# Optimization experiments

Hardware: AMD Instinct MI355X
Metric: run time of the kernel (lower is better)

The kernel has to match this reference:

```python
import jax, jax.numpy as jnp
import numpy as np

NUM_GRAPHS = 1024
DIM = 64
IN_DIM = 25
PROC_STEPS = 3


def setup_inputs() -> dict:
    key = jax.random.key(0)
    ks = jax.random.split(key, 14)
    N, E = 100000, 1600000
    s = 0.1
    x = jax.random.normal(ks[0], (N, IN_DIM), jnp.float32)
    edge_index = jax.random.randint(ks[1], (2, E), 0, N, dtype=jnp.int64)
    batch = jnp.sort(jax.random.randint(ks[2], (N,), 0, NUM_GRAPHS, dtype=jnp.int64))
    return {
        "x": x,
        "edge_index": edge_index,
        "batch": batch,
        # lin0: 25 -> 64
        "lin0_W": jax.random.normal(ks[3], (IN_DIM, DIM), jnp.float32) * s,
        "lin0_b": jnp.zeros((DIM,), jnp.float32),
        # GINConv nn: 64 -> 64
        "gin_W": jax.random.normal(ks[4], (DIM, DIM), jnp.float32) * s,
        "gin_b": jnp.zeros((DIM,), jnp.float32),
        # Set2Set LSTM: input 2*dim -> hidden dim, torch gate order (i, f, g, o)
        "W_ih": jax.random.normal(ks[5], (4 * DIM, 2 * DIM), jnp.float32) * s,
        "W_hh": jax.random.normal(ks[6], (4 * DIM, DIM), jnp.float32) * s,
        "b_ih": jnp.zeros((4 * DIM,), jnp.float32),
        "b_hh": jnp.zeros((4 * DIM,), jnp.float32),
        # lin1: 128 -> 64, lin2: 64 -> 1
        "lin1_W": jax.random.normal(ks[7], (2 * DIM, DIM), jnp.float32) * s,
        "lin1_b": jnp.zeros((DIM,), jnp.float32),
        "lin2_W": jax.random.normal(ks[8], (DIM, 1), jnp.float32) * s,
        "lin2_b": jnp.zeros((1,), jnp.float32),
    }


def reference(x, edge_index, batch, lin0_W, lin0_b, gin_W, gin_b,
              W_ih, W_hh, b_ih, b_hh, lin1_W, lin1_b, lin2_W, lin2_b):
    N = x.shape[0]
    B = NUM_GRAPHS
    # lin0 + relu
    h0 = jax.nn.relu(x @ lin0_W + lin0_b)  # [N, 64]
    # GINConv (eps=0): out = nn((1+eps)*x + sum_{j in N(i)} x_j), then relu
    src, dst = edge_index[0], edge_index[1]
    aggr = jax.ops.segment_sum(h0[src], dst, num_segments=N)  # scatter-add [N, 64]
    h1 = jax.nn.relu((h0 + aggr) @ gin_W + gin_b)  # [N, 64]
    # Set2Set pooling: 3 steps of LSTM + softmax attention over each graph
    q_star = jnp.zeros((B, 2 * DIM), h1.dtype)
    h = jnp.zeros((B, DIM), h1.dtype)
    c = jnp.zeros((B, DIM), h1.dtype)
    for _ in range(PROC_STEPS):
        gates = q_star @ W_ih.T + h @ W_hh.T + b_ih + b_hh  # [B, 4*64]
        i_g, f_g, g_g, o_g = jnp.split(gates, 4, axis=-1)
        c = jax.nn.sigmoid(f_g) * c + jax.nn.sigmoid(i_g) * jnp.tanh(g_g)
        h = jax.nn.sigmoid(o_g) * jnp.tanh(c)
        q = h  # query [B, 64]
        e = jnp.sum(h1 * q[batch], axis=-1)  # [N]
        e_max = jax.ops.segment_max(e, batch, num_segments=B)
        a_un = jnp.exp(e - e_max[batch])
        denom = jax.ops.segment_sum(a_un, batch, num_segments=B)
        denom = jnp.where(denom == 0, 1.0, denom)
        a = a_un / denom[batch]  # per-graph softmax over nodes
        r = jax.ops.segment_sum(a[:, None] * h1, batch, num_segments=B)  # [B, 64]
        q_star = jnp.concatenate([q, r], axis=-1)  # [B, 128]
    out = jax.nn.relu(q_star @ lin1_W + lin1_b)
    out = out @ lin2_W + lin2_b  # [B, 1]
    return out.reshape(-1)
```

## Files before the change

### kernel.cpp

```cpp
#include <hip/hip_runtime.h>
#include <hip/hip_fp16.h>
#include <math.h>

#define DIM 64
#define IN_DIM 25
#define B_GRAPHS 1024
#define STEPS 3
#define MAXDEG 64
#define GPB 2
#define VCAP 16
#define BSHIFT 7
#define NBUCK_MAX 1024
#define BCAP 3072
#define CHUNK_A 4096

typedef _Float16 half8 __attribute__((ext_vector_type(8)));
typedef float    f32x4 __attribute__((ext_vector_type(4)));

__device__ __forceinline__ float wave_sum(float v) {
    #pragma unroll
    for (int o = 32; o > 0; o >>= 1) v += __shfl_xor(v, o, 64);
    return v;
}

__global__ void prepA_kernel(const int* __restrict__ ei, int E,
                             int* __restrict__ gcur,
                             unsigned* __restrict__ arena, int nbuck) {
    __shared__ int hist[NBUCK_MAX];
    int tid = threadIdx.x;
    for (int t = tid; t < nbuck; t += 256) hist[t] = 0;
    __syncthreads();
    int e0 = blockIdx.x * CHUNK_A;
    int dstr[16], lofs[16];
    #pragma unroll
    for (int k = 0; k < 16; ++k) {
        int e = e0 + k * 256 + tid;
        dstr[k] = -1;
        if (e < E) {
            int d = ei[E + e];
            dstr[k] = d;
            lofs[k] = atomicAdd(&hist[d >> BSHIFT], 1);
        }
    }
    __syncthreads();
    for (int t = tid; t < nbuck; t += 256)
        hist[t] = atomicAdd(&gcur[t], hist[t]);
    __syncthreads();
    #pragma unroll
    for (int k = 0; k < 16; ++k) {
        int d = dstr[k];
        if (d >= 0) {
            int e = e0 + k * 256 + tid;
            unsigned src = (unsigned)ei[e];
            int bk = d >> BSHIFT;
            int pos = hist[bk] + lofs[k];
            if (pos < BCAP)
                arena[(size_t)bk * BCAP + pos] =
                    (src << BSHIFT) | (unsigned)(d & ((1 << BSHIFT) - 1));
        }
    }
}

__global__ void prepB_kernel(const float* __restrict__ x,
                             const float* __restrict__ W,
                             const float* __restrict__ b,
                             __half* __restrict__ h0h,
                             const int* __restrict__ batch, int N,
                             const unsigned* __restrict__ arena,
                             const int* __restrict__ gcur,
                             int* __restrict__ cnt, int* __restrict__ csr,
                             int* __restrict__ startb, int* __restrict__ endb,
                             int nbuck, int nbL) {
    int bi = blockIdx.x;
    if (bi < nbuck) {
        int tid = threadIdx.x;
        __shared__ int cur[1 << BSHIFT];
        __shared__ int stage[(1 << BSHIFT) * MAXDEG];
        for (int t = tid; t < (1 << BSHIFT); t += 256) cur[t] = 0;
        __syncthreads();
        int nE = gcur[bi];
        if (nE > BCAP) nE = BCAP;
        int base = bi << BSHIFT;
        const unsigned* ap = arena + (size_t)bi * BCAP;
        for (int i = tid; i < nE; i += 256) {
            unsigned pk = ap[i];
            int dl  = pk & ((1 << BSHIFT) - 1);
            int src = pk >> BSHIFT;
            int pos = atomicAdd(&cur[dl], 1);
            if (pos < MAXDEG) {
                int slot = (pos & 3) * 16 + (pos >> 2);
                stage[dl * MAXDEG + slot] = src;
            }
        }
        __syncthreads();
        int rows = N - base;
        if (rows > (1 << BSHIFT)) rows = 1 << BSHIFT;
        if (rows < 0) rows = 0;
        const int4* s4 = (const int4*)stage;
        int4* g4 = (int4*)(csr + (size_t)base * MAXDEG);
        for (int f = tid; f < rows * 16; f += 256) g4[f] = s4[f];
        for (int t = tid; t < rows; t += 256)
            cnt[base + t] = cur[t] < MAXDEG ? cur[t] : MAXDEG;
    } else if (bi < nbuck + nbL) {
        int grp  = threadIdx.x >> 6;
        int lane = threadIdx.x & 63;
        int n = (bi - nbuck) * 4 + grp;
        if (n >= N) return;
        float acc = b[lane];
        const float* xr = x + (size_t)n * IN_DIM;
        #pragma unroll
        for (int k = 0; k < IN_DIM; ++k)
            acc += xr[k] * W[k * DIM + lane];
        h0h[(size_t)n * DIM + lane] = __float2half(fmaxf(acc, 0.f));
    } else {
        int i = (bi - nbuck - nbL) * 256 + threadIdx.x;
        if (i >= N) return;
        int g = batch[i];
        if (i == 0) {
            startb[g] = 0;
        } else if (batch[i - 1] != g) {
            startb[g] = i;
            endb[batch[i - 1]] = i;
        }
        if (i == N - 1) endb[g] = N;
    }
}

__global__ void gin_gather_kernel(const __half* __restrict__ h0h,
                                  const int* __restrict__ cnt,
                                  const int* __restrict__ csr,
                                  const float* __restrict__ W,
                                  const float* __restrict__ bias,
                                  __half* __restrict__ h1h, int N) {
    int wid  = threadIdx.x >> 6;
    int lane = threadIdx.x & 63;
    int sub  = lane & 15;
    int quad = lane >> 4;
    int nbase = blockIdx.x * 16;
    __shared__ __align__(16) __half agg[16][72];

    half8 bfrag0, bfrag1;
    {
        int cb = wid * 16 + sub;
        #pragma unroll
        for (int j = 0; j < 8; ++j) {
            bfrag0[j] = (_Float16)W[(quad * 8 + j) * DIM + cb];
            bfrag1[j] = (_Float16)W[(32 + quad * 8 + j) * DIM + cb];
        }
    }
    float bias_l = bias[wid * 16 + sub];

    #pragma unroll
    for (int t = 0; t < 4; ++t) {
        int n = nbase + t * 4 + wid;
        if (n < N) {
            int d = cnt[n];
            const int4* crow = (const int4*)(csr + (size_t)n * MAXDEG + quad * 16);
            int4 c0 = crow[0];
            float4 a0 = {0.f, 0.f, 0.f, 0.f};
            float4 a1 = {0.f, 0.f, 0.f, 0.f};

            bool v0 = (0 + quad) < d,  v1 = (4 + quad) < d;
            bool v2 = (8 + quad) < d,  v3 = (12 + quad) < d;
            int i0 = v0 ? c0.x : 0, i1 = v1 ? c0.y : 0;
            int i2 = v2 ? c0.z : 0, i3 = v3 ? c0.w : 0;
            uint2 r0 = *(const uint2*)(h0h + (size_t)i0 * DIM + 4 * sub);
            uint2 r1 = *(const uint2*)(h0h + (size_t)i1 * DIM + 4 * sub);
            uint2 r2 = *(const uint2*)(h0h + (size_t)i2 * DIM + 4 * sub);
            uint2 r3 = *(const uint2*)(h0h + (size_t)i3 * DIM + 4 * sub);
            #define ACC8(r, v, A)                                              \
                if (v) {                                                       \
                    __half2 ua = *reinterpret_cast<__half2*>(&(r).x);          \
                    __half2 ub = *reinterpret_cast<__half2*>(&(r).y);          \
                    float2 fa = __half22float2(ua), fb = __half22float2(ub);   \
                    A.x += fa.x; A.y += fa.y; A.z += fb.x; A.w += fb.y;        \
                }
            ACC8(r0, v0, a0) ACC8(r1, v1, a1) ACC8(r2, v2, a0) ACC8(r3, v3, a1)

            if (d > 16) {
                int4 c1 = crow[1];
                bool v4 = (16 + quad) < d, v5 = (20 + quad) < d;
                bool v6 = (24 + quad) < d, v7 = (28 + quad) < d;
                int i4 = v4 ? c1.x : 0, i5 = v5 ? c1.y : 0;
                int i6 = v6 ? c1.z : 0, i7 = v7 ? c1.w : 0;
                uint2 r4 = *(const uint2*)(h0h + (size_t)i4 * DIM + 4 * sub);
                uint2 r5 = *(const uint2*)(h0h + (size_t)i5 * DIM + 4 * sub);
                uint2 r6 = *(const uint2*)(h0h + (size_t)i6 * DIM + 4 * sub);
                uint2 r7 = *(const uint2*)(h0h + (size_t)i7 * DIM + 4 * sub);
                ACC8(r4, v4, a0) ACC8(r5, v5, a1) ACC8(r6, v6, a0) ACC8(r7, v7, a1)
            }
            if (d > 32) {
                int4 c2 = crow[2];
                int4 c3 = crow[3];
                bool w0 = (32 + quad) < d, w1 = (36 + quad) < d;
                bool w2 = (40 + quad) < d, w3 = (44 + quad) < d;
                bool w4 = (48 + quad) < d, w5 = (52 + quad) < d;
                bool w6 = (56 + quad) < d, w7 = (60 + quad) < d;
                int k0 = w0 ? c2.x : 0, k1 = w1 ? c2.y : 0;
                int k2 = w2 ? c2.z : 0, k3 = w3 ? c2.w : 0;
                int k4 = w4 ? c3.x : 0, k5 = w5 ? c3.y : 0;
                int k6 = w6 ? c3.z : 0, k7 = w7 ? c3.w : 0;
                uint2 t0 = *(const uint2*)(h0h + (size_t)k0 * DIM + 4 * sub);
                uint2 t1 = *(const uint2*)(h0h + (size_t)k1 * DIM + 4 * sub);
                uint2 t2 = *(const uint2*)(h0h + (size_t)k2 * DIM + 4 * sub);
                uint2 t3 = *(const uint2*)(h0h + (size_t)k3 * DIM + 4 * sub);
                uint2 t4 = *(const uint2*)(h0h + (size_t)k4 * DIM + 4 * sub);
                uint2 t5 = *(const uint2*)(h0h + (size_t)k5 * DIM + 4 * sub);
                uint2 t6 = *(const uint2*)(h0h + (size_t)k6 * DIM + 4 * sub);
                uint2 t7 = *(const uint2*)(h0h + (size_t)k7 * DIM + 4 * sub);
                ACC8(t0, w0, a0) ACC8(t1, w1, a1) ACC8(t2, w2, a0) ACC8(t3, w3, a1)
                ACC8(t4, w4, a0) ACC8(t5, w5, a1) ACC8(t6, w6, a0) ACC8(t7, w7, a1)
            }
            #undef ACC8

            float4 a;
            a.x = a0.x + a1.x; a.y = a0.y + a1.y;
            a.z = a0.z + a1.z; a.w = a0.w + a1.w;
            a.x += __shfl_xor(a.x, 16, 64); a.y += __shfl_xor(a.y, 16, 64);
            a.z += __shfl_xor(a.z, 16, 64); a.w += __shfl_xor(a.w, 16, 64);
            a.x += __shfl_xor(a.x, 32, 64); a.y += __shfl_xor(a.y, 32, 64);
            a.z += __shfl_xor(a.z, 32, 64); a.w += __shfl_xor(a.w, 32, 64);
            if (quad == 0) {
                const __half2* p = (const __half2*)(h0h + (size_t)n * DIM + 4 * sub);
                float2 f0 = __half22float2(p[0]), f1 = __half22float2(p[1]);
                a.x += f0.x; a.y += f0.y; a.z += f1.x; a.w += f1.y;
                __half2* dp = (__half2*)&agg[t * 4 + wid][4 * sub];
                dp[0] = __floats2half2_rn(a.x, a.y);
                dp[1] = __floats2half2_rn(a.z, a.w);
            }
        }
    }
    __syncthreads();

    half8 afrag0 = *(const half8*)&agg[sub][quad * 8];
    half8 afrag1 = *(const half8*)&agg[sub][32 + quad * 8];
    f32x4 acc = {0.f, 0.f, 0.f, 0.f};
    acc = __builtin_amdgcn_mfma_f32_16x16x32_f16(afrag0, bfrag0, acc, 0, 0, 0);
    acc = __builtin_amdgcn_mfma_f32_16x16x32_f16(afrag1, bfrag1, acc, 0, 0, 0);
    #pragma unroll
    for (int r = 0; r < 4; ++r) {
        int n = nbase + quad * 4 + r;
        if (n < N) {
            float v = fmaxf(acc[r] + bias_l, 0.f);
            h1h[(size_t)n * DIM + wid * 16 + sub] = __float2half(v);
        }
    }
}

__global__ __launch_bounds__(256)
void set2set_fused_kernel(const __half* __restrict__ h1h,
                          const float* __restrict__ W_ih,
                          const float* __restrict__ W_hh,
                          const float* __restrict__ b_ih,
                          const float* __restrict__ b_hh,
                          const int* __restrict__ startb,
                          const int* __restrict__ endb,
                          const float* __restrict__ lin1_W,
                          const float* __restrict__ lin1_b,
                          const float* __restrict__ lin2_W,
                          const float* __restrict__ lin2_b,
                          float* __restrict__ out) {
    int g0  = blockIdx.x * GPB;
    int tid = threadIdx.x;
    __shared__ __align__(16) float qsbuf[GPB][2 * DIM];
    __shared__ float csbuf[GPB][DIM];
    __shared__ float gatesL[GPB][4 * DIM];
    __shared__ float pmax[GPB][2];
    __shared__ float pden[GPB][2];
    __shared__ __align__(16) float4 pr[GPB][2][16];

    int wid  = tid >> 6;
    int myg  = wid >> 1;
    int wh   = wid & 1;
    int lane = tid & 63;
    int stg  = startb[g0 + myg];
    int cntg = endb[g0 + myg] - stg;
    if (cntg < 0) cntg = 0;

    for (int f = tid; f < GPB * 2 * DIM; f += 256) ((float*)qsbuf)[f] = 0.f;
    for (int f = tid; f < GPB * DIM; f += 256) ((float*)csbuf)[f] = 0.f;
    float bias_t = b_ih[tid] + b_hh[tid];
    __syncthreads();

    int sub   = lane & 15;
    int jslot = lane >> 4;
    int i0    = wh * 4 + jslot;

    for (int step = 0; step < STEPS; ++step) {
        {
            float a0 = bias_t, a1 = bias_t;
            const float4* wi = (const float4*)(W_ih + (size_t)tid * 2 * DIM);
            const float4* q0 = (const float4*)qsbuf[0];
            const float4* q1 = (const float4*)qsbuf[1];
            #pragma unroll 8
            for (int k = 0; k < 2 * DIM / 4; ++k) {
                float4 w = wi[k];
                float4 v0 = q0[k], v1 = q1[k];
                a0 += w.x * v0.x + w.y * v0.y + w.z * v0.z + w.w * v0.w;
                a1 += w.x * v1.x + w.y * v1.y + w.z * v1.z + w.w * v1.w;
            }
            const float4* wh4 = (const float4*)(W_hh + (size_t)tid * DIM);
            #pragma unroll 8
            for (int k = 0; k < DIM / 4; ++k) {
                float4 w = wh4[k];
                float4 v0 = q0[k], v1 = q1[k];
                a0 += w.x * v0.x + w.y * v0.y + w.z * v0.z + w.w * v0.w;
                a1 += w.x * v1.x + w.y * v1.y + w.z * v1.z + w.w * v1.w;
            }
            gatesL[0][tid] = a0; gatesL[1][tid] = a1;
        }
        __syncthreads();
        if (tid < GPB * DIM) {
            int g = tid >> 6, d = tid & 63;
            float ig = gatesL[g][d];
            float fg = gatesL[g][DIM + d];
            float gg = gatesL[g][2 * DIM + d];
            float og = gatesL[g][3 * DIM + d];
            float si = 1.f / (1.f + __expf(-ig));
            float sf = 1.f / (1.f + __expf(-fg));
            float so = 1.f / (1.f + __expf(-og));
            float cn = sf * csbuf[g][d] + si * tanhf(gg);
            float hn = so * tanhf(cn);
            csbuf[g][d] = cn;
            qsbuf[g][d] = hn;
        }
        __syncthreads();

        const float4 q4 = *(const float4*)(&qsbuf[myg][4 * sub]);

        float  pc[VCAP];
        float4 vc[VCAP];
        float gmax = -INFINITY;
        #pragma unroll
        for (int it = 0; it < VCAP; ++it) {
            int i = i0 + it * 8;
            bool vd = i < cntg;
            int r = vd ? (stg + i) : stg;
            const __half2* p = (const __half2*)(h1h + (size_t)r * DIM + 4 * sub);
            float2 f0 = __half22float2(p[0]), f1 = __half22float2(p[1]);
            float4 v; v.x = f0.x; v.y = f0.y; v.z = f1.x; v.w = f1.y;
            float pd = v.x * q4.x + v.y * q4.y + v.z * q4.z + v.w * q4.w;
            pd += __shfl_xor(pd, 1, 64);
            pd += __shfl_xor(pd, 2, 64);
            pd += __shfl_xor(pd, 4, 64);
            pd += __shfl_xor(pd, 8, 64);
            pd = vd ? pd : -INFINITY;
            pc[it] = pd;
            vc[it] = v;
            gmax = fmaxf(gmax, pd);
        }
        for (int i = i0 + VCAP * 8; i < cntg; i += 8) {
            const __half2* p =
                (const __half2*)(h1h + (size_t)(stg + i) * DIM + 4 * sub);
            float2 f0 = __half22float2(p[0]), f1 = __half22float2(p[1]);
            float pd = f0.x * q4.x + f0.y * q4.y + f1.x * q4.z + f1.y * q4.w;
            pd += __shfl_xor(pd, 1, 64);
            pd += __shfl_xor(pd, 2, 64);
            pd += __shfl_xor(pd, 4, 64);
            pd += __shfl_xor(pd, 8, 64);
            gmax = fmaxf(gmax, pd);
        }
        gmax = fmaxf(gmax, __shfl_xor(gmax, 16, 64));
        gmax = fmaxf(gmax, __shfl_xor(gmax, 32, 64));
        if (lane == 0) pmax[myg][wh] = gmax;
        __syncthreads();
        float m = fmaxf(fmaxf(pmax[myg][0], pmax[myg][1]), -1e30f);

        float4 racc = {0.f, 0.f, 0.f, 0.f};
        float den = 0.f;
        #pragma unroll
        for (int it = 0; it < VCAP; ++it) {
            float w = __expf(pc[it] - m);
            if (sub == 0) den += w;
            racc.x += w * vc[it].x; racc.y += w * vc[it].y;
            racc.z += w * vc[it].z; racc.w += w * vc[it].w;
        }
        for (int i = i0 + VCAP * 8; i < cntg; i += 8) {
            const __half2* p =
                (const __half2*)(h1h + (size_t)(stg + i) * DIM + 4 * sub);
            float2 f0 = __half22float2(p[0]), f1 = __half22float2(p[1]);
            float pd = f0.x * q4.x + f0.y * q4.y + f1.x * q4.z + f1.y * q4.w;
            pd += __shfl_xor(pd, 1, 64);
            pd += __shfl_xor(pd, 2, 64);
            pd += __shfl_xor(pd, 4, 64);
            pd += __shfl_xor(pd, 8, 64);
            float w = __expf(pd - m);
            if (sub == 0) den += w;
            racc.x += w * f0.x; racc.y += w * f0.y;
            racc.z += w * f1.x; racc.w += w * f1.y;
        }
        racc.x += __shfl_xor(racc.x, 16, 64); racc.y += __shfl_xor(racc.y, 16, 64);
        racc.z += __shfl_xor(racc.z, 16, 64); racc.w += __shfl_xor(racc.w, 16, 64);
        racc.x += __shfl_xor(racc.x, 32, 64); racc.y += __shfl_xor(racc.y, 32, 64);
        racc.z += __shfl_xor(racc.z, 32, 64); racc.w += __shfl_xor(racc.w, 32, 64);
        den += __shfl_xor(den, 16, 64);
        den += __shfl_xor(den, 32, 64);
        if (jslot == 0) pr[myg][wh][sub] = racc;
        if (lane == 0) pden[myg][wh] = den;
        __syncthreads();
        if (wh == 0 && jslot == 0) {
            float4 rA = pr[myg][0][sub];
            float4 rB = pr[myg][1][sub];
            float dt = pden[myg][0] + pden[myg][1];
            if (dt == 0.f) dt = 1.f;
            float4 rv;
            rv.x = (rA.x + rB.x) / dt; rv.y = (rA.y + rB.y) / dt;
            rv.z = (rA.z + rB.z) / dt; rv.w = (rA.w + rB.w) / dt;
            *(float4*)(&qsbuf[myg][DIM + 4 * sub]) = rv;
        }
        __syncthreads();
    }

    if (wh == 0) {
        float acc = lin1_b[lane];
        const float* qv = qsbuf[myg];
        #pragma unroll 8
        for (int k = 0; k < 2 * DIM; ++k)
            acc += qv[k] * lin1_W[k * DIM + lane];
        acc = fmaxf(acc, 0.f);
        float v = acc * lin2_W[lane];
        v = wave_sum(v);
        if (lane == 0) out[g0 + myg] = v + lin2_b[0];
    }
}

extern "C" void kernel_launch(void* const* d_in, const int* in_sizes, int n_in,
                              void* d_out, int out_size, void* d_ws, size_t ws_size,
                              hipStream_t stream) {
    const float* x      = (const float*)d_in[0];
    const int*   ei     = (const int*)d_in[1];
    const int*   batch  = (const int*)d_in[2];
    const float* lin0_W = (const float*)d_in[3];
    const float* lin0_b = (const float*)d_in[4];
    const float* gin_W  = (const float*)d_in[5];
    const float* gin_b  = (const float*)d_in[6];
    const float* W_ih   = (const float*)d_in[7];
    const float* W_hh   = (const float*)d_in[8];
    const float* b_ih   = (const float*)d_in[9];
    const float* b_hh   = (const float*)d_in[10];
    const float* lin1_W = (const float*)d_in[11];
    const float* lin1_b = (const float*)d_in[12];
    const float* lin2_W = (const float*)d_in[13];
    const float* lin2_b = (const float*)d_in[14];
    float* out = (float*)d_out;

    const int N = in_sizes[2];
    const int E = in_sizes[1] / 2;

    char* ws = (char*)d_ws;
    size_t off = 0;
    auto take = [&](size_t bytes) -> char* {
        char* p = ws + off;
        off += (bytes + 255) & ~(size_t)255;
        return p;
    };
    int nbuck = (N + (1 << BSHIFT) - 1) >> BSHIFT;

    __half*   h0h   = (__half*)take((size_t)N * DIM * 2);
    __half*   h1h   = (__half*)take((size_t)N * DIM * 2);
    int*      csr   = (int*)take((size_t)N * MAXDEG * 4);
    unsigned* arena = (unsigned*)take((size_t)nbuck * BCAP * 4);
    int*      cnt   = (int*)take((size_t)N * 4);
    int* startb = (int*)take((size_t)B_GRAPHS * 4);
    int* endb   = (int*)take((size_t)B_GRAPHS * 4);
    int* gcur   = (int*)take((size_t)NBUCK_MAX * 4);
    size_t zero_bytes = (size_t)((char*)gcur - (char*)startb) + NBUCK_MAX * 4;
    hipMemsetAsync(startb, 0, zero_bytes, stream);

    int nb4   = (N + 3) / 4;
    int nb16  = (N + 15) / 16;
    int nb256 = (N + 255) / 256;
    int fillB = (E + CHUNK_A - 1) / CHUNK_A;

    hipLaunchKernelGGL(prepA_kernel, dim3(fillB), dim3(256), 0, stream,
                       ei, E, gcur, arena, nbuck);
    hipLaunchKernelGGL(prepB_kernel, dim3(nbuck + nb4 + nb256), dim3(256), 0, stream,
                       x, lin0_W, lin0_b, h0h, batch, N,
                       arena, gcur, cnt, csr, startb, endb, nbuck, nb4);
    hipLaunchKernelGGL(gin_gather_kernel, dim3(nb16), dim3(256), 0, stream,
                       h0h, cnt, csr, gin_W, gin_b, h1h, N);
    hipLaunchKernelGGL(set2set_fused_kernel, dim3(B_GRAPHS / GPB), dim3(256), 0, stream,
                       h1h, W_ih, W_hh, b_ih, b_hh, startb, endb,
                       lin1_W, lin1_b, lin2_W, lin2_b, out);
}
```

Baseline: 262.3 us.

## Fuse CSR build into GIN gather and merge edge bucketing with lin0

```diff
diff --git a/kernel.cpp b/kernel.cpp
--- a/kernel.cpp
+++ b/kernel.cpp
@@ -23,88 +23,55 @@
     return v;
 }
 
-__global__ void prepA_kernel(const int* __restrict__ ei, int E,
-                             int* __restrict__ gcur,
-                             unsigned* __restrict__ arena, int nbuck) {
-    __shared__ int hist[NBUCK_MAX];
-    int tid = threadIdx.x;
-    for (int t = tid; t < nbuck; t += 256) hist[t] = 0;
-    __syncthreads();
-    int e0 = blockIdx.x * CHUNK_A;
-    int dstr[16], lofs[16];
-    #pragma unroll
-    for (int k = 0; k < 16; ++k) {
-        int e = e0 + k * 256 + tid;
-        dstr[k] = -1;
-        if (e < E) {
-            int d = ei[E + e];
-            dstr[k] = d;
-            lofs[k] = atomicAdd(&hist[d >> BSHIFT], 1);
-        }
-    }
-    __syncthreads();
-    for (int t = tid; t < nbuck; t += 256)
-        hist[t] = atomicAdd(&gcur[t], hist[t]);
-    __syncthreads();
-    #pragma unroll
-    for (int k = 0; k < 16; ++k) {
-        int d = dstr[k];
-        if (d >= 0) {
-            int e = e0 + k * 256 + tid;
-            unsigned src = (unsigned)ei[e];
-            int bk = d >> BSHIFT;
-            int pos = hist[bk] + lofs[k];
-            if (pos < BCAP)
-                arena[(size_t)bk * BCAP + pos] =
-                    (src << BSHIFT) | (unsigned)(d & ((1 << BSHIFT) - 1));
-        }
-    }
-}
-
-__global__ void prepB_kernel(const float* __restrict__ x,
+__global__ void prepA_kernel(const float* __restrict__ x,
                              const float* __restrict__ W,
                              const float* __restrict__ b,
                              __half* __restrict__ h0h,
+                             const int* __restrict__ ei, int E,
                              const int* __restrict__ batch, int N,
-                             const unsigned* __restrict__ arena,
-                             const int* __restrict__ gcur,
-                             int* __restrict__ cnt, int* __restrict__ csr,
+                             int* __restrict__ gcur,
+                             unsigned* __restrict__ arena,
                              int* __restrict__ startb, int* __restrict__ endb,
-                             int nbuck, int nbL) {
+                             int fillB, int nbL, int nbuck) {
     int bi = blockIdx.x;
-    if (bi < nbuck) {
+    if (bi < fillB) {
+        __shared__ int hist[NBUCK_MAX];
         int tid = threadIdx.x;
-        __shared__ int cur[1 << BSHIFT];
-        __shared__ int stage[(1 << BSHIFT) * MAXDEG];
-        for (int t = tid; t < (1 << BSHIFT); t += 256) cur[t] = 0;
-        __syncthreads();
-        int nE = gcur[bi];
-        if (nE > BCAP) nE = BCAP;
-        int base = bi << BSHIFT;
-        const unsigned* ap = arena + (size_t)bi * BCAP;
-        for (int i = tid; i < nE; i += 256) {
-            unsigned pk = ap[i];
-            int dl  = pk & ((1 << BSHIFT) - 1);
-            int src = pk >> BSHIFT;
-            int pos = atomicAdd(&cur[dl], 1);
-            if (pos < MAXDEG) {
-                int slot = (pos & 3) * 16 + (pos >> 2);
-                stage[dl * MAXDEG + slot] = src;
-            }
-        }
-        __syncthreads();
-        int rows = N - base;
-        if (rows > (1 << BSHIFT)) rows = 1 << BSHIFT;
-        if (rows < 0) rows = 0;
-        const int4* s4 = (const int4*)stage;
-        int4* g4 = (int4*)(csr + (size_t)base * MAXDEG);
-        for (int f = tid; f < rows * 16; f += 256) g4[f] = s4[f];
-        for (int t = tid; t < rows; t += 256)
-            cnt[base + t] = cur[t] < MAXDEG ? cur[t] : MAXDEG;
-    } else if (bi < nbuck + nbL) {
+        for (int t = tid; t < nbuck; t += 256) hist[t] = 0;
+        __syncthreads();
+        int e0 = bi * CHUNK_A;
+        int dstr[16], lofs[16];
+        #pragma unroll
+        for (int k = 0; k < 16; ++k) {
+            int e = e0 + k * 256 + tid;
+            dstr[k] = -1;
+            if (e < E) {
+                int d = ei[E + e];
+                dstr[k] = d;
+                lofs[k] = atomicAdd(&hist[d >> BSHIFT], 1);
+            }
+        }
+        __syncthreads();
+        for (int t = tid; t < nbuck; t += 256)
+            hist[t] = atomicAdd(&gcur[t], hist[t]);
+        __syncthreads();
+        #pragma unroll
+        for (int k = 0; k < 16; ++k) {
+            int d = dstr[k];
+            if (d >= 0) {
+                int e = e0 + k * 256 + tid;
+                unsigned src = (unsigned)ei[e];
+                int bk = d >> BSHIFT;
+                int pos = hist[bk] + lofs[k];
+                if (pos < BCAP)
+                    arena[(size_t)bk * BCAP + pos] =
+                        (src << BSHIFT) | (unsigned)(d & ((1 << BSHIFT) - 1));
+            }
+        }
+    } else if (bi < fillB + nbL) {
         int grp  = threadIdx.x >> 6;
         int lane = threadIdx.x & 63;
-        int n = (bi - nbuck) * 4 + grp;
+        int n = (bi - fillB) * 4 + grp;
         if (n >= N) return;
         float acc = b[lane];
         const float* xr = x + (size_t)n * IN_DIM;
@@ -113,7 +80,7 @@
             acc += xr[k] * W[k * DIM + lane];
         h0h[(size_t)n * DIM + lane] = __float2half(fmaxf(acc, 0.f));
     } else {
-        int i = (bi - nbuck - nbL) * 256 + threadIdx.x;
+        int i = (bi - fillB - nbL) * 256 + threadIdx.x;
         if (i >= N) return;
         int g = batch[i];
         if (i == 0) {
@@ -126,18 +93,26 @@
     }
 }
 
-__global__ void gin_gather_kernel(const __half* __restrict__ h0h,
-                                  const int* __restrict__ cnt,
-                                  const int* __restrict__ csr,
-                                  const float* __restrict__ W,
-                                  const float* __restrict__ bias,
-                                  __half* __restrict__ h1h, int N) {
-    int wid  = threadIdx.x >> 6;
-    int lane = threadIdx.x & 63;
+__global__ void gin_fused_kernel(const __half* __restrict__ h0h,
+                                 const unsigned* __restrict__ arena,
+                                 const int* __restrict__ gcur,
+                                 const float* __restrict__ W,
+                                 const float* __restrict__ bias,
+                                 __half* __restrict__ h1h, int N) {
+    int bk   = blockIdx.x;
+    int tid  = threadIdx.x;
+    int wid  = tid >> 6;
+    int lane = tid & 63;
     int sub  = lane & 15;
     int quad = lane >> 4;
-    int nbase = blockIdx.x * 16;
+    __shared__ int cur[1 << BSHIFT];
+    __shared__ int stage[(1 << BSHIFT) * MAXDEG];
     __shared__ __align__(16) __half agg[16][72];
+
+    int base = bk << BSHIFT;
+    int rows = N - base;
+    if (rows > (1 << BSHIFT)) rows = 1 << BSHIFT;
+    if (rows < 0) rows = 0;
 
     half8 bfrag0, bfrag1;
     {
@@ -150,100 +125,126 @@
     }
     float bias_l = bias[wid * 16 + sub];
 
-    #pragma unroll
-    for (int t = 0; t < 4; ++t) {
-        int n = nbase + t * 4 + wid;
-        if (n < N) {
-            int d = cnt[n];
-            const int4* crow = (const int4*)(csr + (size_t)n * MAXDEG + quad * 16);
-            int4 c0 = crow[0];
-            float4 a0 = {0.f, 0.f, 0.f, 0.f};
-            float4 a1 = {0.f, 0.f, 0.f, 0.f};
-
-            bool v0 = (0 + quad) < d,  v1 = (4 + quad) < d;
-            bool v2 = (8 + quad) < d,  v3 = (12 + quad) < d;
-            int i0 = v0 ? c0.x : 0, i1 = v1 ? c0.y : 0;
-            int i2 = v2 ? c0.z : 0, i3 = v3 ? c0.w : 0;
-            uint2 r0 = *(const uint2*)(h0h + (size_t)i0 * DIM + 4 * sub);
-            uint2 r1 = *(const uint2*)(h0h + (size_t)i1 * DIM + 4 * sub);
-            uint2 r2 = *(const uint2*)(h0h + (size_t)i2 * DIM + 4 * sub);
-            uint2 r3 = *(const uint2*)(h0h + (size_t)i3 * DIM + 4 * sub);
-            #define ACC8(r, v, A)                                              \
-                if (v) {                                                       \
-                    __half2 ua = *reinterpret_cast<__half2*>(&(r).x);          \
-                    __half2 ub = *reinterpret_cast<__half2*>(&(r).y);          \
-                    float2 fa = __half22float2(ua), fb = __half22float2(ub);   \
-                    A.x += fa.x; A.y += fa.y; A.z += fb.x; A.w += fb.y;        \
+    for (int t = tid; t < (1 << BSHIFT); t += 256) cur[t] = 0;
+    __syncthreads();
+    int nE = gcur[bk];
+    if (nE > BCAP) nE = BCAP;
+    const unsigned* ap = arena + (size_t)bk * BCAP;
+    for (int i = tid; i < nE; i += 256) {
+        unsigned pk = ap[i];
+        int dl  = pk & ((1 << BSHIFT) - 1);
+        int src = pk >> BSHIFT;
+        int pos = atomicAdd(&cur[dl], 1);
+        if (pos < MAXDEG) {
+            int slot = (pos & 3) * 16 + (pos >> 2);
+            stage[dl * MAXDEG + slot] = src;
+        }
+    }
+    __syncthreads();
+
+    for (int stt = 0; stt < 8; ++stt) {
+        int r0 = stt * 16;
+        if (r0 >= rows) break;
+        #pragma unroll
+        for (int t = 0; t < 4; ++t) {
+            int rloc = r0 + t * 4 + wid;
+            if (rloc < rows) {
+                int n = base + rloc;
+                int d = cur[rloc];
+                if (d > MAXDEG) d = MAXDEG;
+                const int4* crow = (const int4*)(stage + rloc * MAXDEG + quad * 16);
+                int4 c0 = crow[0];
+                float4 a0 = {0.f, 0.f, 0.f, 0.f};
+                float4 a1 = {0.f, 0.f, 0.f, 0.f};
+
+                bool v0 = (0 + quad) < d,  v1 = (4 + quad) < d;
+                bool v2 = (8 + quad) < d,  v3 = (12 + quad) < d;
+                int i0 = v0 ? c0.x : 0, i1 = v1 ? c0.y : 0;
+                int i2 = v2 ? c0.z : 0, i3 = v3 ? c0.w : 0;
+                uint2 r0v = *(const uint2*)(h0h + (size_t)i0 * DIM + 4 * sub);
+                uint2 r1v = *(const uint2*)(h0h + (size_t)i1 * DIM + 4 * sub);
+                uint2 r2v = *(const uint2*)(h0h + (size_t)i2 * DIM + 4 * sub);
+                uint2 r3v = *(const uint2*)(h0h + (size_t)i3 * DIM + 4 * sub);
+                #define ACC8(r, v, A)                                          \
+                    if (v) {                                                   \
+                        __half2 ua = *reinterpret_cast<__half2*>(&(r).x);      \
+                        __half2 ub = *reinterpret_cast<__half2*>(&(r).y);      \
+                        float2 fa = __half22float2(ua), fb = __half22float2(ub);\
+                        A.x += fa.x; A.y += fa.y; A.z += fb.x; A.w += fb.y;    \
+                    }
+                ACC8(r0v, v0, a0) ACC8(r1v, v1, a1) ACC8(r2v, v2, a0) ACC8(r3v, v3, a1)
+
+                if (d > 16) {
+                    int4 c1 = crow[1];
+                    bool v4 = (16 + quad) < d, v5 = (20 + quad) < d;
+                    bool v6 = (24 + quad) < d, v7 = (28 + quad) < d;
+                    int i4 = v4 ? c1.x : 0, i5 = v5 ? c1.y : 0;
+                    int i6 = v6 ? c1.z : 0, i7 = v7 ? c1.w : 0;
+                    uint2 r4v = *(const uint2*)(h0h + (size_t)i4 * DIM + 4 * sub);
+                    uint2 r5v = *(const uint2*)(h0h + (size_t)i5 * DIM + 4 * sub);
+                    uint2 r6v = *(const uint2*)(h0h + (size_t)i6 * DIM + 4 * sub);
+                    uint2 r7v = *(const uint2*)(h0h + (size_t)i7 * DIM + 4 * sub);
+                    ACC8(r4v, v4, a0) ACC8(r5v, v5, a1)
+                    ACC8(r6v, v6, a0) ACC8(r7v, v7, a1)
                 }
-            ACC8(r0, v0, a0) ACC8(r1, v1, a1) ACC8(r2, v2, a0) ACC8(r3, v3, a1)
-
-            if (d > 16) {
-                int4 c1 = crow[1];
-                bool v4 = (16 + quad) < d, v5 = (20 + quad) < d;
-                bool v6 = (24 + quad) < d, v7 = (28 + quad) < d;
-                int i4 = v4 ? c1.x : 0, i5 = v5 ? c1.y : 0;
-                int i6 = v6 ? c1.z : 0, i7 = v7 ? c1.w : 0;
-                uint2 r4 = *(const uint2*)(h0h + (size_t)i4 * DIM + 4 * sub);
-                uint2 r5 = *(const uint2*)(h0h + (size_t)i5 * DIM + 4 * sub);
-                uint2 r6 = *(const uint2*)(h0h + (size_t)i6 * DIM + 4 * sub);
-                uint2 r7 = *(const uint2*)(h0h + (size_t)i7 * DIM + 4 * sub);
-                ACC8(r4, v4, a0) ACC8(r5, v5, a1) ACC8(r6, v6, a0) ACC8(r7, v7, a1)
-            }
-            if (d > 32) {
-                int4 c2 = crow[2];
-                int4 c3 = crow[3];
-                bool w0 = (32 + quad) < d, w1 = (36 + quad) < d;
-                bool w2 = (40 + quad) < d, w3 = (44 + quad) < d;
-                bool w4 = (48 + quad) < d, w5 = (52 + quad) < d;
-                bool w6 = (56 + quad) < d, w7 = (60 + quad) < d;
-                int k0 = w0 ? c2.x : 0, k1 = w1 ? c2.y : 0;
-                int k2 = w2 ? c2.z : 0, k3 = w3 ? c2.w : 0;
-                int k4 = w4 ? c3.x : 0, k5 = w5 ? c3.y : 0;
-                int k6 = w6 ? c3.z : 0, k7 = w7 ? c3.w : 0;
-                uint2 t0 = *(const uint2*)(h0h + (size_t)k0 * DIM + 4 * sub);
-                uint2 t1 = *(const uint2*)(h0h + (size_t)k1 * DIM + 4 * sub);
-                uint2 t2 = *(const uint2*)(h0h + (size_t)k2 * DIM + 4 * sub);
-                uint2 t3 = *(const uint2*)(h0h + (size_t)k3 * DIM + 4 * sub);
-                uint2 t4 = *(const uint2*)(h0h + (size_t)k4 * DIM + 4 * sub);
-                uint2 t5 = *(const uint2*)(h0h + (size_t)k5 * DIM + 4 * sub);
-                uint2 t6 = *(const uint2*)(h0h + (size_t)k6 * DIM + 4 * sub);
-                uint2 t7 = *(const uint2*)(h0h + (size_t)k7 * DIM + 4 * sub);
-                ACC8(t0, w0, a0) ACC8(t1, w1, a1) ACC8(t2, w2, a0) ACC8(t3, w3, a1)
-                ACC8(t4, w4, a0) ACC8(t5, w5, a1) ACC8(t6, w6, a0) ACC8(t7, w7, a1)
-            }
-            #undef ACC8
-
-            float4 a;
-            a.x = a0.x + a1.x; a.y = a0.y + a1.y;
-            a.z = a0.z + a1.z; a.w = a0.w + a1.w;
-            a.x += __shfl_xor(a.x, 16, 64); a.y += __shfl_xor(a.y, 16, 64);
-            a.z += __shfl_xor(a.z, 16, 64); a.w += __shfl_xor(a.w, 16, 64);
-            a.x += __shfl_xor(a.x, 32, 64); a.y += __shfl_xor(a.y, 32, 64);
-            a.z += __shfl_xor(a.z, 32, 64); a.w += __shfl_xor(a.w, 32, 64);
-            if (quad == 0) {
-                const __half2* p = (const __half2*)(h0h + (size_t)n * DIM + 4 * sub);
-                float2 f0 = __half22float2(p[0]), f1 = __half22float2(p[1]);
-                a.x += f0.x; a.y += f0.y; a.z += f1.x; a.w += f1.y;
-                __half2* dp = (__half2*)&agg[t * 4 + wid][4 * sub];
-                dp[0] = __floats2half2_rn(a.x, a.y);
-                dp[1] = __floats2half2_rn(a.z, a.w);
-            }
-        }
-    }
-    __syncthreads();
-
-    half8 afrag0 = *(const half8*)&agg[sub][quad * 8];
-    half8 afrag1 = *(const half8*)&agg[sub][32 + quad * 8];
-    f32x4 acc = {0.f, 0.f, 0.f, 0.f};
-    acc = __builtin_amdgcn_mfma_f32_16x16x32_f16(afrag0, bfrag0, acc, 0, 0, 0);
-    acc = __builtin_amdgcn_mfma_f32_16x16x32_f16(afrag1, bfrag1, acc, 0, 0, 0);
-    #pragma unroll
-    for (int r = 0; r < 4; ++r) {
-        int n = nbase + quad * 4 + r;
-        if (n < N) {
-            float v = fmaxf(acc[r] + bias_l, 0.f);
-            h1h[(size_t)n * DIM + wid * 16 + sub] = __float2half(v);
-        }
+                if (d > 32) {
+                    int4 c2 = crow[2];
+                    int4 c3 = crow[3];
+                    bool w0 = (32 + quad) < d, w1 = (36 + quad) < d;
+                    bool w2 = (40 + quad) < d, w3 = (44 + quad) < d;
+                    bool w4 = (48 + quad) < d, w5 = (52 + quad) < d;
+                    bool w6 = (56 + quad) < d, w7 = (60 + quad) < d;
+                    int k0 = w0 ? c2.x : 0, k1 = w1 ? c2.y : 0;
+                    int k2 = w2 ? c2.z : 0, k3 = w3 ? c2.w : 0;
+                    int k4 = w4 ? c3.x : 0, k5 = w5 ? c3.y : 0;
+                    int k6 = w6 ? c3.z : 0, k7 = w7 ? c3.w : 0;
+                    uint2 t0 = *(const uint2*)(h0h + (size_t)k0 * DIM + 4 * sub);
+                    uint2 t1 = *(const uint2*)(h0h + (size_t)k1 * DIM + 4 * sub);
+                    uint2 t2 = *(const uint2*)(h0h + (size_t)k2 * DIM + 4 * sub);
+                    uint2 t3 = *(const uint2*)(h0h + (size_t)k3 * DIM + 4 * sub);
+                    uint2 t4 = *(const uint2*)(h0h + (size_t)k4 * DIM + 4 * sub);
+                    uint2 t5 = *(const uint2*)(h0h + (size_t)k5 * DIM + 4 * sub);
+                    uint2 t6 = *(const uint2*)(h0h + (size_t)k6 * DIM + 4 * sub);
+                    uint2 t7 = *(const uint2*)(h0h + (size_t)k7 * DIM + 4 * sub);
+                    ACC8(t0, w0, a0) ACC8(t1, w1, a1) ACC8(t2, w2, a0) ACC8(t3, w3, a1)
+                    ACC8(t4, w4, a0) ACC8(t5, w5, a1) ACC8(t6, w6, a0) ACC8(t7, w7, a1)
+                }
+                #undef ACC8
+
+                float4 a;
+                a.x = a0.x + a1.x; a.y = a0.y + a1.y;
+                a.z = a0.z + a1.z; a.w = a0.w + a1.w;
+                a.x += __shfl_xor(a.x, 16, 64); a.y += __shfl_xor(a.y, 16, 64);
+                a.z += __shfl_xor(a.z, 16, 64); a.w += __shfl_xor(a.w, 16, 64);
+                a.x += __shfl_xor(a.x, 32, 64); a.y += __shfl_xor(a.y, 32, 64);
+                a.z += __shfl_xor(a.z, 32, 64); a.w += __shfl_xor(a.w, 32, 64);
+                if (quad == 0) {
+                    const __half2* p =
+                        (const __half2*)(h0h + (size_t)n * DIM + 4 * sub);
+                    float2 f0 = __half22float2(p[0]), f1 = __half22float2(p[1]);
+                    a.x += f0.x; a.y += f0.y; a.z += f1.x; a.w += f1.y;
+                    __half2* dp = (__half2*)&agg[t * 4 + wid][4 * sub];
+                    dp[0] = __floats2half2_rn(a.x, a.y);
+                    dp[1] = __floats2half2_rn(a.z, a.w);
+                }
+            }
+        }
+        __syncthreads();
+
+        half8 afrag0 = *(const half8*)&agg[sub][quad * 8];
+        half8 afrag1 = *(const half8*)&agg[sub][32 + quad * 8];
+        f32x4 acc = {0.f, 0.f, 0.f, 0.f};
+        acc = __builtin_amdgcn_mfma_f32_16x16x32_f16(afrag0, bfrag0, acc, 0, 0, 0);
+        acc = __builtin_amdgcn_mfma_f32_16x16x32_f16(afrag1, bfrag1, acc, 0, 0, 0);
+        #pragma unroll
+        for (int r = 0; r < 4; ++r) {
+            int rloc = r0 + quad * 4 + r;
+            if (rloc < rows) {
+                float v = fmaxf(acc[r] + bias_l, 0.f);
+                h1h[(size_t)(base + rloc) * DIM + wid * 16 + sub] = __float2half(v);
+            }
+        }
+        __syncthreads();
     }
 }
 
@@ -458,9 +459,7 @@
 
     __half*   h0h   = (__half*)take((size_t)N * DIM * 2);
     __half*   h1h   = (__half*)take((size_t)N * DIM * 2);
-    int*      csr   = (int*)take((size_t)N * MAXDEG * 4);
     unsigned* arena = (unsigned*)take((size_t)nbuck * BCAP * 4);
-    int*      cnt   = (int*)take((size_t)N * 4);
     int* startb = (int*)take((size_t)B_GRAPHS * 4);
     int* endb   = (int*)take((size_t)B_GRAPHS * 4);
     int* gcur   = (int*)take((size_t)NBUCK_MAX * 4);
@@ -468,17 +467,14 @@
     hipMemsetAsync(startb, 0, zero_bytes, stream);
 
     int nb4   = (N + 3) / 4;
-    int nb16  = (N + 15) / 16;
     int nb256 = (N + 255) / 256;
     int fillB = (E + CHUNK_A - 1) / CHUNK_A;
 
-    hipLaunchKernelGGL(prepA_kernel, dim3(fillB), dim3(256), 0, stream,
-                       ei, E, gcur, arena, nbuck);
-    hipLaunchKernelGGL(prepB_kernel, dim3(nbuck + nb4 + nb256), dim3(256), 0, stream,
-                       x, lin0_W, lin0_b, h0h, batch, N,
-                       arena, gcur, cnt, csr, startb, endb, nbuck, nb4);
-    hipLaunchKernelGGL(gin_gather_kernel, dim3(nb16), dim3(256), 0, stream,
-                       h0h, cnt, csr, gin_W, gin_b, h1h, N);
+    hipLaunchKernelGGL(prepA_kernel, dim3(fillB + nb4 + nb256), dim3(256), 0, stream,
+                       x, lin0_W, lin0_b, h0h, ei, E, batch, N,
+                       gcur, arena, startb, endb, fillB, nb4, nbuck);
+    hipLaunchKernelGGL(gin_fused_kernel, dim3(nbuck), dim3(256), 0, stream,
+                       h0h, arena, gcur, gin_W, gin_b, h1h, N);
     hipLaunchKernelGGL(set2set_fused_kernel, dim3(B_GRAPHS / GPB), dim3(256), 0, stream,
                        h1h, W_ih, W_hh, b_ih, b_hh, startb, endb,
                        lin1_W, lin1_b, lin2_W, lin2_b, out);
```

Result: faster. 256.3 us (-2.3%).
